# Optimization experiments

Hardware: AMD Instinct MI355X
Metric: run time of the kernel (lower is better)

The kernel has to match this reference:

```python
import jax, jax.numpy as jnp
import numpy as np

B, S, F_IN, H = 128, 512, 64, 512
EPS = 1e-5  # torch BatchNorm1d default eps


def setup_inputs() -> dict:
    key = jax.random.key(0)
    ks = jax.random.split(key, 20)
    stdv = 1.0 / np.sqrt(H)
    u = lambda k, shape: jax.random.uniform(k, shape, jnp.float32, -stdv, stdv)
    return {
        "input_data": jax.random.normal(ks[0], (B, S, F_IN), jnp.float32),
        # MCLSTM params
        "W": u(ks[1], (F_IN, 4 * H + 5)),
        "U": u(ks[2], (H, 4 * H + 5)),
        "kernel1": u(ks[3], (1, 5 * H)),
        "bias": u(ks[4], (4 * H + 5,)),
        "bias1": u(ks[5], (2 * H,)),
        "rw1": u(ks[6], (H, H // 2)), "rb1": u(ks[7], (H // 2,)),
        "rw2": u(ks[8], (H // 2, H // 4)), "rb2": u(ks[9], (H // 4,)),
        "rbng": jnp.ones((H // 4,), jnp.float32), "rbnb": jnp.zeros((H // 4,), jnp.float32),
        "rw3": u(ks[10], (H // 4, 1)), "rb3": u(ks[11], (1,)),
        # domain classifier head (shared across c1..c5)
        "dw1": u(ks[12], (H, H // 2)), "db1": u(ks[13], (H // 2,)),
        "dbng": jnp.ones((H // 2,), jnp.float32), "dbnb": jnp.zeros((H // 2,), jnp.float32),
        "dw2": u(ks[14], (H // 2, 2)), "db2": u(ks[15], (2,)),
        "alpha": 1,
    }


def _batchnorm(x, g, b):
    # training-mode BatchNorm1d: biased batch stats
    m = jnp.mean(x, axis=0)
    v = jnp.var(x, axis=0)
    return (x - m) / jnp.sqrt(v + EPS) * g + b


def _mclstm_last(x, W, U, kernel1, bias, bias1):
    """Run the MCLSTM recurrence, returning last-step (h, c, c1..c5, d).
    Only the final timestep of each returned sequence is consumed by DANNModel,
    so we carry the per-step values instead of materializing [B,S,H] stacks."""
    bs = x.shape[0]
    s1, s2 = bias1[:H], bias1[H:2 * H]
    k = kernel1.reshape(5, H)  # kernel_1..kernel_5, each [H]

    def step(carry, x_t):
        h, c = carry[0], carry[1]
        gates = x_t @ W + h @ U + bias  # [B, 4H+5]
        i = jax.nn.sigmoid(gates[:, :H])
        f = jax.nn.sigmoid(gates[:, H:2 * H])
        g = jnp.tanh(gates[:, 2 * H:3 * H])
        o = jax.nn.sigmoid(gates[:, 3 * H:4 * H])
        d = jax.nn.softmax(jnp.tanh(gates[:, 4 * H:]), axis=1)  # [B,5]
        c1 = jnp.tanh(g)          # double tanh, faithful to source
        c5 = c
        c3 = f * c + i * g
        c2 = s2 * c3 + (1 - s2) * c1
        c4 = s1 * c3 + (1 - s1) * c5
        # torch.mm(d_j, kernel_j) is an outer product [B,1]x[1,H]
        c_new = ((d[:, 0:1] * k[0]) * c1 + (d[:, 1:2] * k[1]) * c2 +
                 (d[:, 2:3] * k[2]) * c3 + (d[:, 3:4] * k[3]) * c4 +
                 (d[:, 4:5] * k[4]) * c5)
        h_new = o * jnp.tanh(c_new)
        return (h_new, c_new, c1, c2, c3, c4, c5, d), None

    z = jnp.zeros((bs, H), x.dtype)
    init = (z, z, z, z, z, z, z, jnp.zeros((bs, 5), x.dtype))
    carry, _ = jax.lax.scan(step, init, jnp.swapaxes(x, 0, 1))
    return carry


def reference(input_data, W, U, kernel1, bias, bias1,
              rw1, rb1, rw2, rb2, rbng, rbnb, rw3, rb3,
              dw1, db1, dbng, dbnb, dw2, db2, alpha):
    h, c, c1, c2, c3, c4, c5, d = _mclstm_last(input_data, W, U, kernel1, bias, bias1)

    r = jax.nn.relu(h @ rw1 + rb1)
    r = jax.nn.relu(r @ rw2 + rb2)
    r = _batchnorm(r, rbng, rbnb)
    rul = r @ rw3 + rb3

    # domain classifier (ReverseLayerF is identity in forward)
    def dom(feat):
        y = jax.nn.relu(feat @ dw1 + db1)
        y = _batchnorm(y, dbng, dbnb)
        return jax.nn.log_softmax(y @ dw2 + db2, axis=1)

    return (rul, dom(c1), dom(c2), dom(c3), dom(c4), dom(c5), d)
```

## Files before the change

### kernel.cpp

```cpp
#include <hip/hip_runtime.h>
#include <hip/hip_bf16.h>
#include <math.h>

#define Bb   128
#define Ss   512
#define Ff   64
#define Hh   512
#define NGc  2053
#define Kk   576

#define OFF_HB    4096
#define OFF_HFIN  528384
#define OFF_CFIN  790528
#define OFF_R1    2101248
#define OFF_R2    2232320
#define OFF_Y1    2297856
#define OFF_MHB   2101248
#define MHB_BYTES 524288

typedef __attribute__((ext_vector_type(8))) short short8;
typedef __attribute__((ext_vector_type(4))) float f32x4;
typedef __attribute__((ext_vector_type(4))) int   i32x4a;

__device__ __forceinline__ unsigned short f2bf(float f) {
    union { float f; unsigned u; } v; v.f = f;
    unsigned r = v.u + 0x7fffu + ((v.u >> 16) & 1u);
    return (unsigned short)(r >> 16);
}

__device__ __forceinline__ float frcp(float x) { return __builtin_amdgcn_rcpf(x); }

__device__ __forceinline__ float ftanh(float x) {
    float ax = fabsf(x);
    float t  = __expf(-2.f * ax);
    float r  = (1.f - t) * frcp(1.f + t);
    return copysignf(r, x);
}
__device__ __forceinline__ float fsig(float x) {
    return frcp(1.f + __expf(-x));
}

#define HL8(T, a, a2)                                                  \
  asm volatile(                                                        \
    "global_load_dwordx4 %0, %8, off sc0 sc1\n\t"                      \
    "global_load_dwordx4 %1, %8, off offset:16 sc0 sc1\n\t"            \
    "global_load_dwordx4 %2, %8, off offset:2048 sc0 sc1\n\t"          \
    "global_load_dwordx4 %3, %8, off offset:2064 sc0 sc1\n\t"          \
    "global_load_dwordx4 %4, %9, off sc0 sc1\n\t"                      \
    "global_load_dwordx4 %5, %9, off offset:16 sc0 sc1\n\t"            \
    "global_load_dwordx4 %6, %9, off offset:2048 sc0 sc1\n\t"          \
    "global_load_dwordx4 %7, %9, off offset:2064 sc0 sc1\n\t"          \
    "s_waitcnt vmcnt(0)"                                               \
    : "=v"(T[0]), "=v"(T[1]), "=v"(T[2]), "=v"(T[3]),                  \
      "=v"(T[4]), "=v"(T[5]), "=v"(T[6]), "=v"(T[7])                   \
    : "v"(a), "v"(a2) : "memory")

#define HL8S(T, a, a2)                                                 \
  asm volatile(                                                        \
    "global_load_dwordx4 %0, %8, off sc0\n\t"                          \
    "global_load_dwordx4 %1, %8, off offset:16 sc0\n\t"                \
    "global_load_dwordx4 %2, %8, off offset:2048 sc0\n\t"              \
    "global_load_dwordx4 %3, %8, off offset:2064 sc0\n\t"              \
    "global_load_dwordx4 %4, %9, off sc0\n\t"                          \
    "global_load_dwordx4 %5, %9, off offset:16 sc0\n\t"                \
    "global_load_dwordx4 %6, %9, off offset:2048 sc0\n\t"              \
    "global_load_dwordx4 %7, %9, off offset:2064 sc0\n\t"              \
    "s_waitcnt vmcnt(0)"                                               \
    : "=v"(T[0]), "=v"(T[1]), "=v"(T[2]), "=v"(T[3]),                  \
      "=v"(T[4]), "=v"(T[5]), "=v"(T[6]), "=v"(T[7])                   \
    : "v"(a), "v"(a2) : "memory")

__global__ __launch_bounds__(256, 1) void mclstm_main(
    const float* __restrict__ xin, const float* __restrict__ Wm,
    const float* __restrict__ Um,  const float* __restrict__ k1,
    const float* __restrict__ bias, const float* __restrict__ bias1,
    float* __restrict__ out, unsigned char* __restrict__ ws)
{
    __shared__ __align__(16) float predG[2][4][16][16][4];
    __shared__ __align__(16) float predD[2][5][16][4];

    const int tid   = threadIdx.x;
    const int bid   = blockIdx.x;
    const int g_id  = bid & 7;
    const int w_id  = bid >> 3;
    const int lane  = tid & 63;
    const int wv    = tid >> 6;
    const int j0    = w_id * 16;
    const int col16 = lane & 15;
    const int quad  = lane >> 4;

    float* hfin = (float*)(ws + OFF_HFIN);
    float* cfin = (float*)(ws + OFF_CFIN);

    short8 Bf[5][5];
#pragma unroll
    for (int i = 0; i < 4; ++i) {
        int kb = (wv * 4 + i) * 32 + quad * 8;
#pragma unroll
        for (int nt = 0; nt < 5; ++nt) {
            int col = (nt < 4) ? (nt * Hh + j0 + col16)
                               : ((col16 < 5) ? (4 * Hh + col16) : -1);
            short8 b;
#pragma unroll
            for (int j = 0; j < 8; ++j) {
                float v = (col >= 0) ? Um[(size_t)(kb + j) * NGc + col] : 0.f;
                b[j] = (short)f2bf(v);
            }
            Bf[1 + i][nt] = b;
        }
    }
    if (wv < 2) {
        int kb = wv * 32 + quad * 8;
#pragma unroll
        for (int nt = 0; nt < 5; ++nt) {
            int col = (nt < 4) ? (nt * Hh + j0 + col16)
                               : ((col16 < 5) ? (4 * Hh + col16) : -1);
            short8 b;
#pragma unroll
            for (int j = 0; j < 8; ++j) {
                float v = (col >= 0) ? Wm[(size_t)(kb + j) * NGc + col] : 0.f;
                b[j] = (short)f2bf(v);
            }
            Bf[0][nt] = b;
        }
    }

    const int rrow = tid >> 4, uu = tid & 15;
    const int u_g  = j0 + uu;
    const float bi = bias[0 * Hh + u_g], bf = bias[1 * Hh + u_g];
    const float bg = bias[2 * Hh + u_g], bo = bias[3 * Hh + u_g];
    float bd[5], kv[5];
#pragma unroll
    for (int c = 0; c < 5; ++c) { bd[c] = bias[4 * Hh + c]; kv[c] = k1[c * Hh + u_g]; }
    const float s1v = bias1[u_g], s2v = bias1[Hh + u_g];
    float cpreg = 0.f;

    const int kb_p = u_g >> 5, kin = u_g & 31;
    const unsigned pub_off = (unsigned)(kb_p * 2048 + (kin >> 3) * 512 + rrow * 32 + (kin & 7) * 4);

    bool use_fast = true;

    __syncthreads();

    for (int t = 0; t < Ss; ++t) {
        char* hcur = (char*)ws + OFF_HB  + (((t & 1) * 8 + g_id) * 32768);
        char* hnxt = (char*)ws + OFF_HB  + ((((t + 1) & 1) * 8 + g_id) * 32768);
        char* mcur = (char*)ws + OFF_MHB + (((t & 1) * 8 + g_id) * 32768);
        char* mnxt = (char*)ws + OFF_MHB + ((((t + 1) & 1) * 8 + g_id) * 32768);
        const int pp = t & 1;

        f32x4 acc[5];
#pragma unroll
        for (int nt = 0; nt < 5; ++nt) { f32x4 z = {0.f, 0.f, 0.f, 0.f}; acc[nt] = z; }

        if (wv < 2) {
            short8 Ax;
            const float* p = xin + ((size_t)(16 * g_id + col16) * Ss + t) * Ff
                           + wv * 32 + quad * 8;
            f32x4 f0 = *(const f32x4*)(p);
            f32x4 f1 = *(const f32x4*)(p + 4);
#pragma unroll
            for (int j = 0; j < 4; ++j) {
                Ax[j]     = (short)f2bf(f0[j]);
                Ax[4 + j] = (short)f2bf(f1[j]);
            }
#pragma unroll
            for (int nt = 0; nt < 5; ++nt)
                acc[nt] = __builtin_amdgcn_mfma_f32_16x16x32_bf16(Ax, Bf[0][nt], acc[nt], 0, 0, 0);
        }

        i32x4a T[8];
        {
            const unsigned expect = (unsigned)t << 16;
            bool got = false;
            if (use_fast) {
                unsigned long long mb = (unsigned long long)
                    (mcur + (wv * 4) * 2048 + quad * 512 + col16 * 32);
                unsigned long long mb2 = mb + 4096;
                const int bound = (t == 1) ? 1024 : 256;
                for (int it = 0; it < bound; ++it) {
                    HL8S(T, mb, mb2);
                    unsigned diff = 0u;
#pragma unroll
                    for (int i = 0; i < 8; ++i)
#pragma unroll
                        for (int j = 0; j < 4; ++j)
                            diff |= ((unsigned)T[i][j]) ^ expect;
                    if (__all((int)((diff >> 16) == 0u))) { got = true; break; }
                }
                if (!got) use_fast = false;
            }
            if (!got) {
                unsigned long long hb = (unsigned long long)
                    (hcur + (wv * 4) * 2048 + quad * 512 + col16 * 32);
                unsigned long long hb2 = hb + 4096;
                for (int it = 0; it < (1 << 22); ++it) {
                    HL8(T, hb, hb2);
                    unsigned diff = 0u;
#pragma unroll
                    for (int i = 0; i < 8; ++i)
#pragma unroll
                        for (int j = 0; j < 4; ++j)
                            diff |= ((unsigned)T[i][j]) ^ expect;
                    if (__all((int)((diff >> 16) == 0u))) break;
                }
            }
        }

#pragma unroll
        for (int i = 0; i < 4; ++i) {
            short8 a;
#pragma unroll
            for (int j = 0; j < 4; ++j) {
                a[j]     = (short)(T[2 * i][j] & 0xFFFF);
                a[4 + j] = (short)(T[2 * i + 1][j] & 0xFFFF);
            }
#pragma unroll
            for (int nt = 0; nt < 5; ++nt)
                acc[nt] = __builtin_amdgcn_mfma_f32_16x16x32_bf16(a, Bf[1 + i][nt], acc[nt], 0, 0, 0);
        }

#pragma unroll
        for (int j = 0; j < 4; ++j) {
            f32x4 g4 = {acc[0][j], acc[1][j], acc[2][j], acc[3][j]};
            *(f32x4*)&predG[pp][wv][quad * 4 + j][col16][0] = g4;
        }
        if (col16 < 5) {
#pragma unroll
            for (int j = 0; j < 4; ++j)
                predD[pp][col16][quad * 4 + j][wv] = acc[4][j];
        }
        __syncthreads();

        {
            f32x4 g4 = {bi, bf, bg, bo};
#pragma unroll
            for (int w = 0; w < 4; ++w) {
                f32x4 p = *(const f32x4*)&predG[pp][w][rrow][uu][0];
                g4 += p;
            }
            float dv[5];
#pragma unroll
            for (int c = 0; c < 5; ++c) {
                f32x4 dp = *(const f32x4*)&predD[pp][c][rrow][0];
                dv[c] = bd[c] + ((dp[0] + dp[1]) + (dp[2] + dp[3]));
            }
            float sden = 0.f;
#pragma unroll
            for (int c = 0; c < 5; ++c) { dv[c] = __expf(ftanh(dv[c])); sden += dv[c]; }
            float inv = frcp(sden);
#pragma unroll
            for (int c = 0; c < 5; ++c) dv[c] *= inv;

            float i_ = fsig(g4[0]);
            float f_ = fsig(g4[1]);
            float g_ = ftanh(g4[2]);
            float o_ = fsig(g4[3]);
            float c1v = ftanh(g_);
            float c5v = cpreg;
            float c3v = f_ * c5v + i_ * g_;
            float c2v = s2v * c3v + (1.f - s2v) * c1v;
            float c4v = s1v * c3v + (1.f - s1v) * c5v;
            float cn = dv[0] * kv[0] * c1v + dv[1] * kv[1] * c2v + dv[2] * kv[2] * c3v
                     + dv[3] * kv[3] * c4v + dv[4] * kv[4] * c5v;
            float hn = o_ * ftanh(cn);
            cpreg = cn;

            if (t < Ss - 1) {
                unsigned word = ((unsigned)(t + 1) << 16) | (unsigned)f2bf(hn);
                *(volatile unsigned*)(mnxt + pub_off) = word;
                __hip_atomic_store((unsigned*)(hnxt + pub_off), word,
                                   __ATOMIC_RELAXED, __HIP_MEMORY_SCOPE_AGENT);
            } else {
                size_t off = (size_t)(16 * g_id + rrow) * Hh + u_g;
                hfin[off] = hn;
                cfin[0 * Bb * Hh + off] = c1v;
                cfin[1 * Bb * Hh + off] = c2v;
                cfin[2 * Bb * Hh + off] = c3v;
                cfin[3 * Bb * Hh + off] = c4v;
                cfin[4 * Bb * Hh + off] = c5v;
                if (w_id == 0 && uu == 0) {
#pragma unroll
                    for (int c = 0; c < 5; ++c)
                        out[1408 + (16 * g_id + rrow) * 5 + c] = dv[c];
                }
            }
        }
    }
}

__global__ __launch_bounds__(256) void stageA(const unsigned char* __restrict__ ws,
    const float* __restrict__ rw1, const float* __restrict__ rb1,
    const float* __restrict__ dw1, const float* __restrict__ db1)
{
    __shared__ float sW[512 * 17];
    const int tid = threadIdx.x;
    const int blk = blockIdx.x;
    const float* hfin = (const float*)(ws + OFF_HFIN);
    const float* cfin = (const float*)(ws + OFF_CFIN);
    float* r1 = (float*)(ws + OFF_R1);
    float* y1 = (float*)(ws + OFF_Y1);

    const float* src; const float* Wm; const float* bv; float* dst; int cblk;
    if (blk < 16) { src = hfin; Wm = rw1; bv = rb1; dst = r1; cblk = blk; }
    else {
        int hd = (blk - 16) >> 4; cblk = (blk - 16) & 15;
        src = cfin + (size_t)hd * Bb * Hh; Wm = dw1; bv = db1;
        dst = y1 + (size_t)hd * Bb * 256;
    }
    for (int e = tid; e < 512 * 16; e += 256) {
        int k = e >> 4, c = e & 15;
        sW[k * 17 + c] = Wm[(size_t)k * 256 + cblk * 16 + c];
    }
    __syncthreads();
    for (int e = tid; e < 128 * 16; e += 256) {
        int r = e >> 4, c = e & 15;
        float a = bv[cblk * 16 + c];
        const float* sp = src + (size_t)r * 512;
        for (int k = 0; k < 512; k += 4) {
            f32x4 h4 = *(const f32x4*)(sp + k);
            a += h4[0] * sW[(k + 0) * 17 + c] + h4[1] * sW[(k + 1) * 17 + c]
               + h4[2] * sW[(k + 2) * 17 + c] + h4[3] * sW[(k + 3) * 17 + c];
        }
        dst[(size_t)r * 256 + cblk * 16 + c] = fmaxf(a, 0.f);
    }
}

__global__ __launch_bounds__(256) void stageB(const unsigned char* __restrict__ ws,
    const float* __restrict__ rw2, const float* __restrict__ rb2)
{
    __shared__ float sW[256 * 17];
    const int tid = threadIdx.x;
    const int cblk = blockIdx.x;
    const float* r1 = (const float*)(ws + OFF_R1);
    float* r2 = (float*)(ws + OFF_R2);
    for (int e = tid; e < 256 * 16; e += 256) {
        int k = e >> 4, c = e & 15;
        sW[k * 17 + c] = rw2[(size_t)k * 128 + cblk * 16 + c];
    }
    __syncthreads();
    for (int e = tid; e < 128 * 16; e += 256) {
        int r = e >> 4, c = e & 15;
        float a = rb2[cblk * 16 + c];
        const float* sp = r1 + (size_t)r * 256;
        for (int k = 0; k < 256; k += 4) {
            f32x4 h4 = *(const f32x4*)(sp + k);
            a += h4[0] * sW[(k + 0) * 17 + c] + h4[1] * sW[(k + 1) * 17 + c]
               + h4[2] * sW[(k + 2) * 17 + c] + h4[3] * sW[(k + 3) * 17 + c];
        }
        r2[(size_t)r * 128 + cblk * 16 + c] = fmaxf(a, 0.f);
    }
}

__global__ __launch_bounds__(256) void stageC(const unsigned char* __restrict__ ws,
    const float* __restrict__ rbng, const float* __restrict__ rbnb,
    const float* __restrict__ rw3,  const float* __restrict__ rb3,
    const float* __restrict__ dbng, const float* __restrict__ dbnb,
    const float* __restrict__ dw2,  const float* __restrict__ db2,
    float* __restrict__ out)
{
    __shared__ float sc[256], sh[256];
    const int tid = threadIdx.x;
    const int blk = blockIdx.x;
    const float* r2 = (const float*)(ws + OFF_R2);
    const float* y1 = (const float*)(ws + OFF_Y1);
    if (blk == 0) {
        if (tid < 128) {
            int c = tid; float s = 0.f, s2 = 0.f;
            for (int r = 0; r < 128; ++r) { float x = r2[r * 128 + c]; s += x; s2 += x * x; }
            float m = s * (1.f / 128.f), v = s2 * (1.f / 128.f) - m * m;
            float sca = rbng[c] * rsqrtf(v + 1e-5f);
            sc[c] = sca; sh[c] = rbnb[c] - m * sca;
        }
        __syncthreads();
        if (tid < 128) {
            int r = tid; float a = rb3[0];
            for (int c = 0; c < 128; ++c)
                a += (r2[r * 128 + c] * sc[c] + sh[c]) * rw3[c];
            out[r] = a;
        }
    } else {
        int hd = blk - 1;
        const float* y = y1 + (size_t)hd * 128 * 256;
        {
            int c = tid; float s = 0.f, s2 = 0.f;
            for (int r = 0; r < 128; ++r) { float x = y[r * 256 + c]; s += x; s2 += x * x; }
            float m = s * (1.f / 128.f), v = s2 * (1.f / 128.f) - m * m;
            float sca = dbng[c] * rsqrtf(v + 1e-5f);
            sc[c] = sca; sh[c] = dbnb[c] - m * sca;
        }
        __syncthreads();
        if (tid < 128) {
            int r = tid;
            float z0 = db2[0], z1 = db2[1];
            for (int c = 0; c < 256; ++c) {
                float yn = y[r * 256 + c] * sc[c] + sh[c];
                z0 += yn * dw2[c * 2 + 0];
                z1 += yn * dw2[c * 2 + 1];
            }
            float mx = fmaxf(z0, z1);
            float ls = mx + logf(__expf(z0 - mx) + __expf(z1 - mx));
            out[128 + hd * 256 + r * 2 + 0] = z0 - ls;
            out[128 + hd * 256 + r * 2 + 1] = z1 - ls;
        }
    }
}

extern "C" void kernel_launch(void* const* d_in, const int* in_sizes, int n_in,
                              void* d_out, int out_size, void* d_ws, size_t ws_size,
                              hipStream_t stream) {
    const float* x    = (const float*)d_in[0];
    const float* Wm   = (const float*)d_in[1];
    const float* Um   = (const float*)d_in[2];
    const float* k1   = (const float*)d_in[3];
    const float* bias = (const float*)d_in[4];
    const float* b1   = (const float*)d_in[5];
    const float* rw1  = (const float*)d_in[6];
    const float* rb1  = (const float*)d_in[7];
    const float* rw2  = (const float*)d_in[8];
    const float* rb2  = (const float*)d_in[9];
    const float* rbng = (const float*)d_in[10];
    const float* rbnb = (const float*)d_in[11];
    const float* rw3  = (const float*)d_in[12];
    const float* rb3  = (const float*)d_in[13];
    const float* dw1  = (const float*)d_in[14];
    const float* db1  = (const float*)d_in[15];
    const float* dbng = (const float*)d_in[16];
    const float* dbnb = (const float*)d_in[17];
    const float* dw2  = (const float*)d_in[18];
    const float* db2  = (const float*)d_in[19];
    (void)in_sizes; (void)n_in; (void)out_size; (void)ws_size;

    hipMemsetAsync(d_ws, 0, OFF_HFIN, stream);
    hipMemsetAsync((char*)d_ws + OFF_MHB, 0, MHB_BYTES, stream);

    mclstm_main<<<256, 256, 0, stream>>>(x, Wm, Um, k1, bias, b1,
                                         (float*)d_out, (unsigned char*)d_ws);
    stageA<<<96, 256, 0, stream>>>((const unsigned char*)d_ws, rw1, rb1, dw1, db1);
    stageB<<<8, 256, 0, stream>>>((const unsigned char*)d_ws, rw2, rb2);
    stageC<<<6, 256, 0, stream>>>((const unsigned char*)d_ws, rbng, rbnb, rw3, rb3,
                                  dbng, dbnb, dw2, db2, (float*)d_out);
}
```

Baseline: 1.356 ms.

## Assign batch groups by XCD at runtime and prefetch next-step input

At kernel start each block reads its hardware XCD id and takes a rank through atomic counters. If all 8 XCDs hold exactly 32 blocks, each batch group is mapped to one XCD, so the per-step h exchange stays within that XCD's shared L2 fast path. Otherwise it falls back to the old blockIdx mapping and skips the fast-path mirror writes. The x_t load for the next step is also issued right after the spin-wait so its latency overlaps the MFMA and gate math, and the fast-path spin bounds are raised. The cost is an extra grid-wide handshake at startup, plus the assumption that all 256 blocks are co-resident.

```diff
diff --git a/kernel.cpp b/kernel.cpp
--- a/kernel.cpp
+++ b/kernel.cpp
@@ -78,19 +78,52 @@
 {
     __shared__ __align__(16) float predG[2][4][16][16][4];
     __shared__ __align__(16) float predD[2][5][16][4];
+    __shared__ unsigned s_role[3];
 
     const int tid   = threadIdx.x;
     const int bid   = blockIdx.x;
-    const int g_id  = bid & 7;
-    const int w_id  = bid >> 3;
     const int lane  = tid & 63;
     const int wv    = tid >> 6;
-    const int j0    = w_id * 16;
     const int col16 = lane & 15;
     const int quad  = lane >> 4;
 
     float* hfin = (float*)(ws + OFF_HFIN);
     float* cfin = (float*)(ws + OFF_CFIN);
+
+    if (tid == 0) {
+        unsigned xcd;
+        asm volatile("s_getreg_b32 %0, hwreg(HW_REG_XCC_ID)" : "=s"(xcd));
+        xcd &= 7u;
+        unsigned* cnt = (unsigned*)ws;
+        unsigned* tot = (unsigned*)(ws + 1024);
+        unsigned* ver = (unsigned*)(ws + 1088);
+        unsigned rank = __hip_atomic_fetch_add(cnt + xcd * 16, 1u,
+                            __ATOMIC_RELAXED, __HIP_MEMORY_SCOPE_AGENT);
+        unsigned n = __hip_atomic_fetch_add(tot, 1u,
+                            __ATOMIC_ACQ_REL, __HIP_MEMORY_SCOPE_AGENT);
+        if (n == 255u) {
+            bool bal = true;
+            for (int i = 0; i < 8; ++i)
+                bal = bal && (__hip_atomic_load(cnt + i * 16, __ATOMIC_RELAXED,
+                                  __HIP_MEMORY_SCOPE_AGENT) == 32u);
+            __hip_atomic_store(ver, bal ? 1u : 2u,
+                               __ATOMIC_RELEASE, __HIP_MEMORY_SCOPE_AGENT);
+        }
+        unsigned V = 0u;
+        for (long it = 0; it < (1L << 26); ++it) {
+            V = __hip_atomic_load(ver, __ATOMIC_ACQUIRE, __HIP_MEMORY_SCOPE_AGENT);
+            if (V) break;
+        }
+        const bool fast = (V == 1u);
+        s_role[0] = fast ? 1u : 0u;
+        s_role[1] = fast ? xcd  : (unsigned)(bid & 7);
+        s_role[2] = fast ? rank : (unsigned)(bid >> 3);
+    }
+    __syncthreads();
+    const int  mode = (int)s_role[0];
+    const int  g_id = (int)s_role[1];
+    const int  w_id = (int)s_role[2];
+    const int  j0   = w_id * 16;
 
     short8 Bf[5][5];
 #pragma unroll
@@ -138,7 +171,14 @@
     const int kb_p = u_g >> 5, kin = u_g & 31;
     const unsigned pub_off = (unsigned)(kb_p * 2048 + (kin >> 3) * 512 + rrow * 32 + (kin & 7) * 4);
 
-    bool use_fast = true;
+    const float* xbase = xin + (size_t)(16 * g_id + col16) * Ss * Ff + wv * 32 + quad * 8;
+    f32x4 xf0 = {0.f, 0.f, 0.f, 0.f}, xf1 = {0.f, 0.f, 0.f, 0.f};
+    if (wv < 2) {
+        xf0 = *(const f32x4*)(xbase);
+        xf1 = *(const f32x4*)(xbase + 4);
+    }
+
+    bool use_fast = (mode != 0);
 
     __syncthreads();
 
@@ -155,14 +195,10 @@
 
         if (wv < 2) {
             short8 Ax;
-            const float* p = xin + ((size_t)(16 * g_id + col16) * Ss + t) * Ff
-                           + wv * 32 + quad * 8;
-            f32x4 f0 = *(const f32x4*)(p);
-            f32x4 f1 = *(const f32x4*)(p + 4);
 #pragma unroll
             for (int j = 0; j < 4; ++j) {
-                Ax[j]     = (short)f2bf(f0[j]);
-                Ax[4 + j] = (short)f2bf(f1[j]);
+                Ax[j]     = (short)f2bf(xf0[j]);
+                Ax[4 + j] = (short)f2bf(xf1[j]);
             }
 #pragma unroll
             for (int nt = 0; nt < 5; ++nt)
@@ -177,7 +213,7 @@
                 unsigned long long mb = (unsigned long long)
                     (mcur + (wv * 4) * 2048 + quad * 512 + col16 * 32);
                 unsigned long long mb2 = mb + 4096;
-                const int bound = (t == 1) ? 1024 : 256;
+                const int bound = (t <= 1) ? 4096 : 1024;
                 for (int it = 0; it < bound; ++it) {
                     HL8S(T, mb, mb2);
                     unsigned diff = 0u;
@@ -205,6 +241,12 @@
                     if (__all((int)((diff >> 16) == 0u))) break;
                 }
             }
+        }
+
+        if (wv < 2 && t + 1 < Ss) {
+            const float* p = xbase + (size_t)(t + 1) * Ff;
+            xf0 = *(const f32x4*)(p);
+            xf1 = *(const f32x4*)(p + 4);
         }
 
 #pragma unroll
@@ -268,7 +310,9 @@
 
             if (t < Ss - 1) {
                 unsigned word = ((unsigned)(t + 1) << 16) | (unsigned)f2bf(hn);
-                *(volatile unsigned*)(mnxt + pub_off) = word;
+                if (mode) {
+                    *(volatile unsigned*)(mnxt + pub_off) = word;
+                }
                 __hip_atomic_store((unsigned*)(hnxt + pub_off), word,
                                    __ATOMIC_RELAXED, __HIP_MEMORY_SCOPE_AGENT);
             } else {
```

New measurement: 2.202 ms. +62.4%, slower.
